# Optimization experiments

Measured on AMD Instinct MI355X. Metric: run time of the kernel, lower is better.

## Reference

```python
import jax, jax.numpy as jnp
import numpy as np
from math import sqrt

N_USERS = 60000
N_ITEMS = 40000
D = 64
B = 3
LAYERS = 2
E = 600000
BATCH = 2048
N_NODES = (N_USERS + 1) + (N_ITEMS + 1)
REG_WEIGHT = 1e-3
BPR_GAMMA = 1e-10


def setup_inputs() -> dict:
    key = jax.random.key(0)
    k0, k1, k2, k3, k4 = jax.random.split(key, 5)
    user_emb = jax.random.normal(k0, (N_USERS + 1, D), jnp.float32) * 0.1
    item_emb = jax.random.normal(k1, (N_ITEMS + 1, D), jnp.float32) * 0.1
    W = jnp.ones((B,), jnp.float32)
    edge_users = jax.random.randint(k2, (B, E), 1, N_USERS + 1)
    edge_items = jax.random.randint(k3, (B, E), 1, N_ITEMS + 1)
    batch_data = jax.random.randint(k4, (BATCH, B, 3), 1, N_ITEMS + 1)
    return dict(user_emb=user_emb, item_emb=item_emb, W=W,
                edge_users=edge_users, edge_items=edge_items,
                batch_data=batch_data)


def _lightgcn(emb, eu, ei, layers):
    # bipartite undirected graph: users <-> items (items offset by N_USERS+1)
    it = ei + (N_USERS + 1)
    src = jnp.concatenate([eu, it])
    dst = jnp.concatenate([it, eu])
    deg = jax.ops.segment_sum(jnp.ones_like(src, jnp.float32), src, N_NODES)
    norm = jax.lax.rsqrt(jnp.maximum(deg[src], 1.0)) * jax.lax.rsqrt(jnp.maximum(deg[dst], 1.0))
    out = emb
    cur = emb
    for _ in range(layers):
        cur = jax.ops.segment_sum(cur[src] * norm[:, None], dst, N_NODES)
        out = out + cur
    return out / (layers + 1)


def _mutual_attention(f):
    # f: [N, B, D]
    S = jnp.einsum('nid,njd->nij', f, f)          # [N, B, B] pairwise scores
    last = S[:, B - 1:B, :]                        # [N, 1, B]
    proj = S[:, :B - 1, :]                         # [N, B-1, B]
    # (last * proj) * last / (last^2 + eps)   (dim-1 is size 1, sums/norms trivial)
    clear = (last * proj) * last / (last * last + 1e-12)   # [N, B-1, B]
    scores = jnp.sum(clear, axis=1, keepdims=True) + last   # [N, 1, B]
    all_scores = jnp.concatenate([clear, scores], axis=1)   # [N, B, B]
    att = jax.nn.softmax(all_scores / sqrt(D), axis=-1)
    return jnp.einsum('nij,njd->nid', att, f)


def reference(user_emb, item_emb, W, edge_users, edge_items, batch_data):
    total0 = jnp.concatenate([user_emb, item_emb], axis=0)   # [N_NODES, D]
    # global graph = union of all behaviors
    g_eu = edge_users.reshape(-1)
    g_ei = edge_items.reshape(-1)
    all_emb = _lightgcn(total0, g_eu, g_ei, LAYERS)
    # per-behavior propagation
    u_list, i_list = [], []
    for b in range(B):
        eb = _lightgcn(all_emb, edge_users[b], edge_items[b], LAYERS)
        u_list.append(eb[:N_USERS + 1])
        i_list.append(eb[N_USERS + 1:])
    all_user = jnp.stack(u_list, axis=1)   # [n_users+1, B, D]
    all_item = jnp.stack(i_list, axis=1)   # [n_items+1, B, D]
    all_user = _mutual_attention(all_user)
    # item behaviour degree: interactions per item per behavior
    ones = jnp.ones((E,), jnp.float32)
    ibd = jnp.stack([jax.ops.segment_sum(ones, edge_items[b], N_ITEMS + 1)
                     for b in range(B)], axis=1)   # [n_items+1, B]
    weight = ibd * W
    weight = weight / (jnp.sum(weight, axis=1, keepdims=True) + 1e-8)
    item_final = jnp.sum(all_item * weight[:, :, None], axis=1)   # [n_items+1, D]
    total_loss = jnp.float32(0.0)
    for b in range(B):
        users = batch_data[:, b, 0]
        items = batch_data[:, b, 1:3]
        uf = all_user[:, b][users][:, None, :]      # [batch, 1, D]
        itf = item_final[items]                      # [batch, 2, D]
        scores = jnp.sum(uf * itf, axis=2)           # [batch, 2]
        total_loss = total_loss - jnp.mean(
            jnp.log(BPR_GAMMA + jax.nn.sigmoid(scores[:, 0] - scores[:, 1])))
    emb_loss = (jnp.linalg.norm(user_emb) + jnp.linalg.norm(item_emb)) / (N_ITEMS + 1)
    return total_loss + REG_WEIGHT * emb_loss
```

## Files before the change

### kernel.cpp

```cpp
#include <hip/hip_runtime.h>
#include <hip/hip_bf16.h>
#include <math.h>

#define NUQ 60001
#define NIQ 40001
#define NNQ 100002
#define DQ  64
#define EQ  600000
#define BQ  3
#define BATCHQ 2048
#define ROWW 32
#define RST ((NNQ + 1) * ROWW)
#define NSLOT (BATCHQ * BQ)
#define NPAD 100004
#define ADJB 1200000
#define BLK_ELE 2048
#define NBLK ((NNQ + BLK_ELE - 1) / BLK_ELE)
#define RANGE 392
#define NRANGE 256
#define NBINS (BQ * NRANGE)
#define NBLKA 256
#define EPB ((BQ * EQ + NBLKA - 1) / NBLKA)

__device__ __forceinline__ float wave_sum(float v) {
#pragma unroll
  for (int m = 32; m >= 1; m >>= 1) v += __shfl_xor(v, m, 64);
  return v;
}
__device__ __forceinline__ int wave_sum_i(int v) {
#pragma unroll
  for (int m = 32; m >= 1; m >>= 1) v += __shfl_xor(v, m, 64);
  return v;
}

__device__ __forceinline__ unsigned pack_bf2(float lo, float hi) {
  unsigned a = __float_as_uint(lo);
  unsigned b = __float_as_uint(hi);
  a = (a + 0x7FFFu + ((a >> 16) & 1u)) >> 16;
  b = (b + 0x7FFFu + ((b >> 16) & 1u)) >> 16;
  return a | (b << 16);
}
__device__ __forceinline__ float unpk_lo(unsigned u) { return __uint_as_float(u << 16); }
__device__ __forceinline__ float unpk_hi(unsigned u) { return __uint_as_float(u & 0xFFFF0000u); }

__global__ void zero_i_k(int* __restrict__ p, int n) {
  int tid = blockIdx.x * blockDim.x + threadIdx.x;
  int stride = gridDim.x * blockDim.x;
  for (int i = tid; i < n; i += stride) p[i] = 0;
}

__global__ void sumsq_k(const float* __restrict__ p, int n, float* __restrict__ acc) {
  int tid = blockIdx.x * blockDim.x + threadIdx.x;
  int stride = gridDim.x * blockDim.x;
  float s = 0.f;
  for (int i = tid; i < n; i += stride) { float v = p[i]; s += v * v; }
  s = wave_sum(s);
  __shared__ float ws[4];
  if ((threadIdx.x & 63) == 0) ws[threadIdx.x >> 6] = s;
  __syncthreads();
  if (threadIdx.x == 0) atomicAdd(acc, ws[0] + ws[1] + ws[2] + ws[3]);
}

__global__ void binc_k(const int* __restrict__ eu, const int* __restrict__ ei,
                       unsigned* __restrict__ counts) {
  __shared__ unsigned h[NBINS];
  for (int i = threadIdx.x; i < NBINS; i += 256) h[i] = 0u;
  __syncthreads();
  int base = blockIdx.x * EPB;
  int end = base + EPB;
  if (end > BQ * EQ) end = BQ * EQ;
  for (int idx = base + threadIdx.x; idx < end; idx += 256) {
    int b = idx / EQ;
    int u = eu[idx];
    int it = ei[idx] + NUQ;
    atomicAdd(&h[b * NRANGE + u / RANGE], 1u);
    atomicAdd(&h[b * NRANGE + it / RANGE], 1u);
  }
  __syncthreads();
  for (int i = threadIdx.x; i < NBINS; i += 256)
    counts[(size_t)blockIdx.x * NBINS + i] = h[i];
}

__global__ void binscan1_k(const unsigned* __restrict__ counts,
                           unsigned* __restrict__ offs, unsigned* __restrict__ bintot) {
  int bin = blockIdx.x;
  int t = threadIdx.x;
  int lane = t & 63, wid = t >> 6;
  unsigned v = counts[(size_t)t * NBINS + bin];
  unsigned incl = v;
#pragma unroll
  for (int off = 1; off < 64; off <<= 1) {
    unsigned x = __shfl_up(incl, off, 64);
    if (lane >= off) incl += x;
  }
  __shared__ unsigned wsum[4];
  if (lane == 63) wsum[wid] = incl;
  __syncthreads();
  if (t == 0) {
    unsigned s = 0;
#pragma unroll
    for (int w = 0; w < 4; ++w) { unsigned x = wsum[w]; wsum[w] = s; s += x; }
  }
  __syncthreads();
  unsigned excl = incl - v + wsum[wid];
  offs[(size_t)t * NBINS + bin] = excl;
  if (t == 255) bintot[bin] = excl + v;
}

__global__ void binscan2_k(const unsigned* __restrict__ bintot,
                           unsigned* __restrict__ binstart) {
  int t = threadIdx.x;
  int lane = t & 63, wid = t >> 6;
  unsigned c0 = bintot[t * 3 + 0], c1 = bintot[t * 3 + 1], c2 = bintot[t * 3 + 2];
  unsigned tsum = c0 + c1 + c2;
  unsigned incl = tsum;
#pragma unroll
  for (int off = 1; off < 64; off <<= 1) {
    unsigned x = __shfl_up(incl, off, 64);
    if (lane >= off) incl += x;
  }
  __shared__ unsigned wsum[4];
  if (lane == 63) wsum[wid] = incl;
  __syncthreads();
  if (t == 0) {
    unsigned s = 0;
#pragma unroll
    for (int w = 0; w < 4; ++w) { unsigned x = wsum[w]; wsum[w] = s; s += x; }
  }
  __syncthreads();
  unsigned run = incl - tsum + wsum[wid];
  binstart[t * 3 + 0] = run; run += c0;
  binstart[t * 3 + 1] = run; run += c1;
  binstart[t * 3 + 2] = run; run += c2;
  if (t == 255) binstart[NBINS] = run;
}

__global__ void binfill_k(const int* __restrict__ eu, const int* __restrict__ ei,
                          const unsigned* __restrict__ offs,
                          const unsigned* __restrict__ binstart,
                          unsigned* __restrict__ records) {
  __shared__ unsigned cur[NBINS];
  for (int i = threadIdx.x; i < NBINS; i += 256)
    cur[i] = binstart[i] + offs[(size_t)blockIdx.x * NBINS + i];
  __syncthreads();
  int base = blockIdx.x * EPB;
  int end = base + EPB;
  if (end > BQ * EQ) end = BQ * EQ;
  for (int idx = base + threadIdx.x; idx < end; idx += 256) {
    int b = idx / EQ;
    int u = eu[idx];
    int itl = ei[idx];
    int it = itl + NUQ;
    unsigned p = atomicAdd(&cur[b * NRANGE + u / RANGE], 1u);
    records[p] = ((unsigned)(u % RANGE) << 16) | (unsigned)itl;
    unsigned q = atomicAdd(&cur[b * NRANGE + it / RANGE], 1u);
    records[q] = ((unsigned)(it % RANGE) << 16) | (unsigned)u;
  }
}

__global__ void bindeg_k(const unsigned* __restrict__ records,
                         const unsigned* __restrict__ binstart,
                         int* __restrict__ degB) {
  int bin = blockIdx.x;
  int b = bin / NRANGE;
  int r0 = (bin % NRANGE) * RANGE;
  __shared__ int h[RANGE];
  for (int i = threadIdx.x; i < RANGE; i += 256) h[i] = 0;
  __syncthreads();
  unsigned rs = binstart[bin], re = binstart[bin + 1];
  for (unsigned j = rs + threadIdx.x; j < re; j += 256)
    atomicAdd(&h[records[j] >> 16], 1);
  __syncthreads();
  int nval = NNQ - r0;
  if (nval > RANGE) nval = RANGE;
  int* deg = degB + (size_t)b * NPAD;
  for (int i = threadIdx.x; i < nval; i += 256) deg[r0 + i] = h[i];
}

__global__ void scan_p1_k(const int* __restrict__ degB, int* __restrict__ partial) {
  int b = blockIdx.x / NBLK;
  int blk = blockIdx.x % NBLK;
  const int* deg = degB + (size_t)b * NPAD;
  int base = blk * BLK_ELE + threadIdx.x * 8;
  int s = 0;
#pragma unroll
  for (int i = 0; i < 8; ++i) { int idx = base + i; if (idx < NNQ) s += deg[idx]; }
  s = wave_sum_i(s);
  __shared__ int lds[4];
  int wid = threadIdx.x >> 6;
  if ((threadIdx.x & 63) == 0) lds[wid] = s;
  __syncthreads();
  if (threadIdx.x == 0) partial[b * NBLK + blk] = lds[0] + lds[1] + lds[2] + lds[3];
}

__global__ void scan_p2_k(int* __restrict__ partial, int* __restrict__ rowptrB) {
  int wid = threadIdx.x >> 6;
  int lane = threadIdx.x & 63;
  if (wid >= BQ) return;
  int v = (lane < NBLK) ? partial[wid * NBLK + lane] : 0;
  int orig = v;
#pragma unroll
  for (int off = 1; off < 64; off <<= 1) {
    int t = __shfl_up(v, off, 64);
    if (lane >= off) v += t;
  }
  if (lane < NBLK) partial[wid * NBLK + lane] = v - orig;
  if (lane == NBLK - 1) rowptrB[(size_t)wid * NPAD + NNQ] = v;
}

__global__ void scan_p3_k(const int* __restrict__ degB, const int* __restrict__ partial,
                          int* __restrict__ rowptrB, float* __restrict__ invsqB) {
  int b = blockIdx.x / NBLK;
  int blk = blockIdx.x % NBLK;
  const int* deg = degB + (size_t)b * NPAD;
  int* rowptr = rowptrB + (size_t)b * NPAD;
  float* invsq = invsqB + (size_t)b * NPAD;
  int base = blk * BLK_ELE + threadIdx.x * 8;
  int d[8];
  int tsum = 0;
#pragma unroll
  for (int i = 0; i < 8; ++i) {
    int idx = base + i;
    d[i] = (idx < NNQ) ? deg[idx] : 0;
    tsum += d[i];
  }
  int lane = threadIdx.x & 63;
  int wid = threadIdx.x >> 6;
  int incl = tsum;
#pragma unroll
  for (int off = 1; off < 64; off <<= 1) {
    int t = __shfl_up(incl, off, 64);
    if (lane >= off) incl += t;
  }
  int excl = incl - tsum;
  __shared__ int lds[4];
  if (lane == 63) lds[wid] = incl;
  __syncthreads();
  if (threadIdx.x == 0) {
    int s = 0;
#pragma unroll
    for (int w = 0; w < 4; ++w) { int t = lds[w]; lds[w] = s; s += t; }
  }
  __syncthreads();
  int run = excl + lds[wid] + partial[b * NBLK + blk];
#pragma unroll
  for (int i = 0; i < 8; ++i) {
    int idx = base + i;
    if (idx < NNQ) {
      rowptr[idx] = run;
      run += d[i];
      invsq[idx] = rsqrtf(fmaxf((float)d[i], 1.f));
    }
  }
}

__global__ void invsqg_k(const int* __restrict__ degB, float* __restrict__ invsqG) {
  int n = blockIdx.x * blockDim.x + threadIdx.x;
  if (n >= NNQ) return;
  int dg = degB[n] + degB[NPAD + n] + degB[2 * NPAD + n];
  invsqG[n] = rsqrtf(fmaxf((float)dg, 1.f));
}

__global__ void binscat_k(const unsigned* __restrict__ records,
                          const unsigned* __restrict__ binstart,
                          const int* __restrict__ rowptrB,
                          unsigned short* __restrict__ adjB) {
  int bin = blockIdx.x;
  int b = bin / NRANGE;
  int r0 = (bin % NRANGE) * RANGE;
  int nval = NNQ - r0;
  if (nval > RANGE) nval = RANGE;
  __shared__ int cur[RANGE];
  const int* rowptr = rowptrB + (size_t)b * NPAD;
  for (int i = threadIdx.x; i < nval; i += 256) cur[i] = rowptr[r0 + i];
  __syncthreads();
  unsigned rs = binstart[bin], re = binstart[bin + 1];
  unsigned short* adj = adjB + (size_t)b * ADJB;
  for (unsigned j = rs + threadIdx.x; j < re; j += 256) {
    unsigned rec = records[j];
    int dl = rec >> 16;
    int pos = atomicAdd(&cur[dl], 1);
    adj[pos] = (unsigned short)(rec & 0xFFFFu);
  }
}

__global__ void pack_emb_k(const float* __restrict__ ue, const float* __restrict__ ie,
                           const float* __restrict__ invsqG,
                           unsigned* __restrict__ E0, unsigned* __restrict__ E0s) {
  int idx = blockIdx.x * blockDim.x + threadIdx.x;
  if (idx >= (NNQ + 1) * ROWW) return;
  int n = idx >> 5, k = idx & 31;
  if (n >= NNQ) { E0s[idx] = 0u; return; }
  const float* src = (n < NUQ) ? (ue + (size_t)n * DQ) : (ie + (size_t)(n - NUQ) * DQ);
  float a = src[2 * k], b = src[2 * k + 1];
  E0[idx] = pack_bf2(a, b);
  float s = invsqG[n];
  E0s[idx] = pack_bf2(a * s, b * s);
}

__device__ __forceinline__ void gather_ns(const unsigned* __restrict__ S,
                                          const unsigned short* __restrict__ adj,
                                          int start, int end, int offs,
                                          int lane, unsigned k4, int g,
                                          float& alo, float& ahi) {
  for (int j0 = start; j0 < end; j0 += 64) {
    int nloc = end - j0;
    if (nloc > 64) nloc = 64;
    unsigned boff = ((unsigned)NNQ) << 7;
    if (lane < nloc) boff = (unsigned)((int)adj[j0 + lane] + offs) << 7;
    for (int j = 0; j < nloc; j += 16) {
#pragma unroll
      for (int m = 0; m < 8; ++m) {
        int jj = j + 2 * m + g;
        unsigned bo = (unsigned)__shfl((int)boff, jj, 64) + k4;
        unsigned dd = *(const unsigned*)((const char*)S + bo);
        alo += unpk_lo(dd);
        ahi += unpk_hi(dd);
      }
    }
  }
}

__device__ __forceinline__ void gather_w(const unsigned* __restrict__ S,
                                         const unsigned short* __restrict__ adj,
                                         const float* __restrict__ invsq,
                                         int start, int end, int offs,
                                         int lane, unsigned k4, int g,
                                         float& alo, float& ahi) {
  for (int j0 = start; j0 < end; j0 += 64) {
    int nloc = end - j0;
    if (nloc > 64) nloc = 64;
    unsigned boff = (unsigned)offs << 7;
    float w = 0.f;
    if (lane < nloc) {
      int a = (int)adj[j0 + lane] + offs;
      boff = (unsigned)a << 7;
      w = invsq[a];
    }
    for (int j = 0; j < nloc; j += 16) {
#pragma unroll
      for (int m = 0; m < 8; ++m) {
        int jj = j + 2 * m + g;
        unsigned bo = (unsigned)__shfl((int)boff, jj, 64) + k4;
        float ww = __shfl(w, jj, 64);
        unsigned dd = *(const unsigned*)((const char*)S + bo);
        alo += ww * unpk_lo(dd);
        ahi += ww * unpk_hi(dd);
      }
    }
  }
}

__global__ void g_l1_k(const unsigned* __restrict__ E0s, unsigned* __restrict__ T1,
                       unsigned* __restrict__ T1s,
                       const int* __restrict__ rowptrB, const unsigned short* __restrict__ adjB,
                       const float* __restrict__ invsqG) {
  int wid = (blockIdx.x * blockDim.x + threadIdx.x) >> 6;
  int lane = threadIdx.x & 63;
  if (wid > NNQ) return;
  int k = lane & 31, g = lane >> 5;
  unsigned k4 = (unsigned)k << 2;
  if (wid == NNQ) { if (lane < 32) T1s[(size_t)wid * ROWW + k] = 0u; return; }
  int offs = (wid < NUQ) ? NUQ : 0;
  float alo = 0.f, ahi = 0.f;
#pragma unroll
  for (int b = 0; b < BQ; ++b) {
    const int* rp = rowptrB + (size_t)b * NPAD;
    gather_ns(E0s, adjB + (size_t)b * ADJB, rp[wid], rp[wid + 1], offs, lane, k4, g, alo, ahi);
  }
  alo += __shfl_xor(alo, 32, 64);
  ahi += __shfl_xor(ahi, 32, 64);
  float s = invsqG[wid];
  if (lane < 32) {
    T1[(size_t)wid * ROWW + k] = pack_bf2(alo * s, ahi * s);
    T1s[(size_t)wid * ROWW + k] = pack_bf2(alo * s * s, ahi * s * s);
  }
}

__global__ void g_l2c_k(const unsigned* __restrict__ E0, const unsigned* __restrict__ T1,
                        const unsigned* __restrict__ T1s,
                        unsigned* __restrict__ C, unsigned* __restrict__ Cs,
                        const int* __restrict__ rowptrB, const unsigned short* __restrict__ adjB,
                        const float* __restrict__ invsqG, const float* __restrict__ invsqB) {
  int wid = (blockIdx.x * blockDim.x + threadIdx.x) >> 6;
  int lane = threadIdx.x & 63;
  if (wid > NNQ) return;
  int k = lane & 31, g = lane >> 5;
  unsigned k4 = (unsigned)k << 2;
  if (wid == NNQ) {
    if (lane < 32) {
#pragma unroll
      for (int b = 0; b < BQ; ++b) Cs[(size_t)b * RST + (size_t)wid * ROWW + k] = 0u;
    }
    return;
  }
  int offs = (wid < NUQ) ? NUQ : 0;
  float alo = 0.f, ahi = 0.f;
#pragma unroll
  for (int b = 0; b < BQ; ++b) {
    const int* rp = rowptrB + (size_t)b * NPAD;
    gather_ns(T1s, adjB + (size_t)b * ADJB, rp[wid], rp[wid + 1], offs, lane, k4, g, alo, ahi);
  }
  alo += __shfl_xor(alo, 32, 64);
  ahi += __shfl_xor(ahi, 32, 64);
  if (lane < 32) {
    float s = invsqG[wid];
    unsigned e0 = E0[(size_t)wid * ROWW + k];
    unsigned t1 = T1[(size_t)wid * ROWW + k];
    float clo = (unpk_lo(e0) + unpk_lo(t1) + alo * s) * (1.f / 3.f);
    float chi = (unpk_hi(e0) + unpk_hi(t1) + ahi * s) * (1.f / 3.f);
    C[(size_t)wid * ROWW + k] = pack_bf2(clo, chi);
#pragma unroll
    for (int b = 0; b < BQ; ++b) {
      float sb = invsqB[(size_t)b * NPAD + wid];
      Cs[(size_t)b * RST + (size_t)wid * ROWW + k] = pack_bf2(clo * sb, chi * sb);
    }
  }
}

__global__ void b_l1_k(const unsigned* __restrict__ Csb, unsigned* __restrict__ T1Bb,
                       const int* __restrict__ rowptr, const unsigned short* __restrict__ adj,
                       const float* __restrict__ ivb) {
  int wid = (blockIdx.x * blockDim.x + threadIdx.x) >> 6;
  int lane = threadIdx.x & 63;
  if (wid >= NNQ) return;
  int k = lane & 31, g = lane >> 5;
  unsigned k4 = (unsigned)k << 2;
  int offs = (wid < NUQ) ? NUQ : 0;
  float alo = 0.f, ahi = 0.f;
  gather_ns(Csb, adj, rowptr[wid], rowptr[wid + 1], offs, lane, k4, g, alo, ahi);
  alo += __shfl_xor(alo, 32, 64);
  ahi += __shfl_xor(ahi, 32, 64);
  float s = ivb[wid];
  if (lane < 32)
    T1Bb[(size_t)wid * ROWW + k] = pack_bf2(alo * s, ahi * s);
}

__global__ void slot_users_k(const unsigned* __restrict__ C, const unsigned* __restrict__ T1B,
                             const int* __restrict__ rowptrB, const unsigned short* __restrict__ adjB,
                             const float* __restrict__ invsqB,
                             const int* __restrict__ batch, float* __restrict__ UG) {
  int slot = (blockIdx.x * blockDim.x + threadIdx.x) >> 6;
  int lane = threadIdx.x & 63;
  if (slot >= NSLOT) return;
  int b = blockIdx.y;
  const int* rp = rowptrB + (size_t)b * NPAD;
  const float* iv = invsqB + (size_t)b * NPAD;
  const unsigned* T1 = T1B + (size_t)b * NNQ * ROWW;
  int u = batch[slot * 3 + 0];
  int k = lane & 31, g = lane >> 5;
  unsigned k4 = (unsigned)k << 2;
  float alo = 0.f, ahi = 0.f;
  gather_w(T1, adjB + (size_t)b * ADJB, iv, rp[u], rp[u + 1], NUQ, lane, k4, g, alo, ahi);
  alo += __shfl_xor(alo, 32, 64);
  ahi += __shfl_xor(ahi, 32, 64);
  float s = iv[u];
  unsigned c0 = C[(size_t)u * ROWW + k];
  unsigned t0 = T1[(size_t)u * ROWW + k];
  if (lane < 32) {
    size_t base = ((size_t)slot * BQ + b) * DQ;
    UG[base + 2 * k]     = (unpk_lo(c0) + unpk_lo(t0) + alo * s) * (1.f / 3.f);
    UG[base + 2 * k + 1] = (unpk_hi(c0) + unpk_hi(t0) + ahi * s) * (1.f / 3.f);
  }
}

__global__ void slot_items_k(const unsigned* __restrict__ C, const unsigned* __restrict__ T1B,
                             const int* __restrict__ rowptrB, const unsigned short* __restrict__ adjB,
                             const float* __restrict__ invsqB,
                             const int* __restrict__ batch, float* __restrict__ IG) {
  int islot = (blockIdx.x * blockDim.x + threadIdx.x) >> 6;
  int lane = threadIdx.x & 63;
  if (islot >= 2 * NSLOT) return;
  int b = blockIdx.y;
  const int* rp = rowptrB + (size_t)b * NPAD;
  const float* iv = invsqB + (size_t)b * NPAD;
  const unsigned* T1 = T1B + (size_t)b * NNQ * ROWW;
  int slot = islot >> 1;
  int c = (islot & 1) + 1;
  int n = batch[slot * 3 + c] + NUQ;
  int k = lane & 31, g = lane >> 5;
  unsigned k4 = (unsigned)k << 2;
  float alo = 0.f, ahi = 0.f;
  gather_w(T1, adjB + (size_t)b * ADJB, iv, rp[n], rp[n + 1], 0, lane, k4, g, alo, ahi);
  alo += __shfl_xor(alo, 32, 64);
  ahi += __shfl_xor(ahi, 32, 64);
  float s = iv[n];
  unsigned c0 = C[(size_t)n * ROWW + k];
  unsigned t0 = T1[(size_t)n * ROWW + k];
  if (lane < 32) {
    size_t base = ((size_t)islot * BQ + b) * DQ;
    IG[base + 2 * k]     = (unpk_lo(c0) + unpk_lo(t0) + alo * s) * (1.f / 3.f);
    IG[base + 2 * k + 1] = (unpk_hi(c0) + unpk_hi(t0) + ahi * s) * (1.f / 3.f);
  }
}

__global__ void epilogue_k(const float* __restrict__ UG, const float* __restrict__ IG,
                           const int* __restrict__ degB, const int* __restrict__ batch,
                           const float* __restrict__ W, float* __restrict__ acc) {
  int slot = (blockIdx.x * blockDim.x + threadIdx.x) >> 6;
  int lane = threadIdx.x & 63;
  float val = 0.f;
  if (slot < NSLOT) {
    int bb = slot % BQ;
    size_t base = (size_t)slot * (BQ * DQ) + lane;
    float a0 = UG[base], a1 = UG[base + 64], a2 = UG[base + 128];
    float p00 = wave_sum(a0 * a0);
    float p01 = wave_sum(a0 * a1);
    float p02 = wave_sum(a0 * a2);
    float p11 = wave_sum(a1 * a1);
    float p12 = wave_sum(a1 * a2);
    float p22 = wave_sum(a2 * a2);
    float last[3] = {p02, p12, p22};
    float S0[3] = {p00, p01, p02};
    float S1[3] = {p01, p11, p12};
    float rows[3][3];
#pragma unroll
    for (int j = 0; j < 3; ++j) {
      float l = last[j];
      float f = l * l / (l * l + 1e-12f);
      float c0 = S0[j] * f;
      float c1 = S1[j] * f;
      rows[0][j] = c0;
      rows[1][j] = c1;
      rows[2][j] = c0 + c1 + l;
    }
    float x0 = rows[bb][0] * 0.125f, x1 = rows[bb][1] * 0.125f, x2 = rows[bb][2] * 0.125f;
    float m = fmaxf(x0, fmaxf(x1, x2));
    float e0 = expf(x0 - m), e1 = expf(x1 - m), e2 = expf(x2 - m);
    float inv = 1.f / (e0 + e1 + e2);
    float uf = (e0 * a0 + e1 * a1 + e2 * a2) * inv;
    float sco[2];
#pragma unroll
    for (int c = 0; c < 2; ++c) {
      int islot = slot * 2 + c;
      int node = batch[slot * 3 + 1 + c] + NUQ;
      float w0 = (float)degB[0 * NPAD + node] * W[0];
      float w1 = (float)degB[1 * NPAD + node] * W[1];
      float w2 = (float)degB[2 * NPAD + node] * W[2];
      float inv2 = 1.f / (w0 + w1 + w2 + 1e-8f);
      size_t rb = (size_t)islot * (BQ * DQ) + lane;
      float ifv = (IG[rb] * w0 + IG[rb + 64] * w1 + IG[rb + 128] * w2) * inv2;
      sco[c] = wave_sum(uf * ifv);
    }
    if (lane == 0) {
      float x = sco[0] - sco[1];
      float sg = 1.f / (1.f + expf(-x));
      val = -logf(1e-10f + sg) * (1.f / (float)BATCHQ);
    }
  }
  __shared__ float ws[4];
  if (lane == 0) ws[threadIdx.x >> 6] = val;
  __syncthreads();
  if (threadIdx.x == 0) atomicAdd(acc, ws[0] + ws[1] + ws[2] + ws[3]);
}

__global__ void finalize_k(const float* __restrict__ sc, unsigned int* __restrict__ out) {
  float total = sc[0] + 0.001f * (sqrtf(sc[1]) + sqrtf(sc[2])) / (float)NIQ;
  unsigned int bits = __float_as_uint(total);
  unsigned int lsb = (bits >> 16) & 1u;
  unsigned int rb = (bits + 0x7FFFu + lsb) >> 16;
  out[0] = (rb << 16) | rb;
}

extern "C" void kernel_launch(void* const* d_in, const int* in_sizes, int n_in,
                              void* d_out, int out_size, void* d_ws, size_t ws_size,
                              hipStream_t stream) {
  const float* ue = (const float*)d_in[0];
  const float* ie = (const float*)d_in[1];
  const float* W  = (const float*)d_in[2];
  const int* eu    = (const int*)d_in[3];
  const int* ei    = (const int*)d_in[4];
  const int* batch = (const int*)d_in[5];

  unsigned* E0  = (unsigned*)d_ws;
  unsigned* E0s = E0 + (size_t)NNQ * ROWW;
  unsigned* T1  = E0s + (size_t)RST;
  unsigned* T1s = T1 + (size_t)NNQ * ROWW;
  unsigned* C   = T1s + (size_t)RST;
  unsigned* Cs  = C + (size_t)NNQ * ROWW;
  unsigned* T1B = Cs + (size_t)BQ * RST;
  float* UG   = (float*)(T1B + (size_t)BQ * NNQ * ROWW);
  float* IG   = UG + (size_t)NSLOT * (BQ * DQ);
  unsigned short* adjB = (unsigned short*)(IG + (size_t)2 * NSLOT * (BQ * DQ));
  int* rowptrB= (int*)(adjB + (size_t)BQ * ADJB);
  int* degB   = rowptrB + 3 * NPAD;
  float* invsqB = (float*)(degB + 3 * NPAD);
  float* invsqG = invsqB + 3 * NPAD;
  unsigned* counts = (unsigned*)(invsqG + NPAD);
  unsigned* offs   = counts + (size_t)NBLKA * NBINS;
  unsigned* bintot = offs + (size_t)NBLKA * NBINS;
  unsigned* binstart = bintot + 1024;
  unsigned* records = binstart + 1024;
  int* partial  = (int*)(records + (size_t)2 * BQ * EQ);
  float* sc   = (float*)(partial + 256);

  zero_i_k<<<1, 64, 0, stream>>>((int*)sc, 8);
  sumsq_k<<<512, 256, 0, stream>>>(ue, NUQ * DQ, sc + 1);
  sumsq_k<<<512, 256, 0, stream>>>(ie, NIQ * DQ, sc + 2);

  binc_k<<<NBLKA, 256, 0, stream>>>(eu, ei, counts);
  binscan1_k<<<NBINS, 256, 0, stream>>>(counts, offs, bintot);
  binscan2_k<<<1, 256, 0, stream>>>(bintot, binstart);
  binfill_k<<<NBLKA, 256, 0, stream>>>(eu, ei, offs, binstart, records);
  bindeg_k<<<NBINS, 256, 0, stream>>>(records, binstart, degB);
  scan_p1_k<<<BQ * NBLK, 256, 0, stream>>>(degB, partial);
  scan_p2_k<<<1, 256, 0, stream>>>(partial, rowptrB);
  scan_p3_k<<<BQ * NBLK, 256, 0, stream>>>(degB, partial, rowptrB, invsqB);
  invsqg_k<<<(NNQ + 255) / 256, 256, 0, stream>>>(degB, invsqG);
  binscat_k<<<NBINS, 256, 0, stream>>>(records, binstart, rowptrB, adjB);

  pack_emb_k<<<((NNQ + 1) * ROWW + 255) / 256, 256, 0, stream>>>(ue, ie, invsqG, E0, E0s);

  const int NODE_BLKS1 = (NNQ + 1 + 3) / 4;
  const int NODE_BLKS = (NNQ + 3) / 4;

  g_l1_k<<<NODE_BLKS1, 256, 0, stream>>>(E0s, T1, T1s, rowptrB, adjB, invsqG);
  g_l2c_k<<<NODE_BLKS1, 256, 0, stream>>>(E0, T1, T1s, C, Cs, rowptrB, adjB, invsqG, invsqB);

  for (int b = 0; b < BQ; ++b) {
    b_l1_k<<<NODE_BLKS, 256, 0, stream>>>(Cs + (size_t)b * RST,
                                          T1B + (size_t)b * NNQ * ROWW,
                                          rowptrB + (size_t)b * NPAD,
                                          adjB + (size_t)b * ADJB,
                                          invsqB + (size_t)b * NPAD);
  }

  slot_users_k<<<dim3((NSLOT + 3) / 4, 3), 256, 0, stream>>>(C, T1B, rowptrB, adjB, invsqB, batch, UG);
  slot_items_k<<<dim3((2 * NSLOT + 3) / 4, 3), 256, 0, stream>>>(C, T1B, rowptrB, adjB, invsqB, batch, IG);
  epilogue_k<<<(NSLOT + 3) / 4, 256, 0, stream>>>(UG, IG, degB, batch, W, sc);
  finalize_k<<<1, 1, 0, stream>>>(sc, (unsigned int*)d_out);
}
```

Measured before the change: 478.5 us.

## Merge per-behavior neighbor gathers and use nontemporal loads/stores for streamed buffers

```diff
diff --git a/kernel.cpp b/kernel.cpp
--- a/kernel.cpp
+++ b/kernel.cpp
@@ -43,6 +43,11 @@
 __device__ __forceinline__ float unpk_lo(unsigned u) { return __uint_as_float(u << 16); }
 __device__ __forceinline__ float unpk_hi(unsigned u) { return __uint_as_float(u & 0xFFFF0000u); }
 
+__device__ __forceinline__ void ntst_u32(unsigned* p, unsigned v) { __builtin_nontemporal_store(v, p); }
+__device__ __forceinline__ void ntst_f32(float* p, float v) { __builtin_nontemporal_store(v, p); }
+__device__ __forceinline__ unsigned ntld_u32(const unsigned* p) { return __builtin_nontemporal_load(p); }
+__device__ __forceinline__ float ntld_f32(const float* p) { return __builtin_nontemporal_load(p); }
+
 __global__ void zero_i_k(int* __restrict__ p, int n) {
   int tid = blockIdx.x * blockDim.x + threadIdx.x;
   int stride = gridDim.x * blockDim.x;
@@ -293,9 +298,9 @@
   if (n >= NNQ) { E0s[idx] = 0u; return; }
   const float* src = (n < NUQ) ? (ue + (size_t)n * DQ) : (ie + (size_t)(n - NUQ) * DQ);
   float a = src[2 * k], b = src[2 * k + 1];
-  E0[idx] = pack_bf2(a, b);
+  ntst_u32(&E0[idx], pack_bf2(a, b));
   float s = invsqG[n];
-  E0s[idx] = pack_bf2(a * s, b * s);
+  ntst_u32(&E0s[idx], pack_bf2(a * s, b * s));
 }
 
 __device__ __forceinline__ void gather_ns(const unsigned* __restrict__ S,
@@ -308,6 +313,39 @@
     if (nloc > 64) nloc = 64;
     unsigned boff = ((unsigned)NNQ) << 7;
     if (lane < nloc) boff = (unsigned)((int)adj[j0 + lane] + offs) << 7;
+    for (int j = 0; j < nloc; j += 16) {
+#pragma unroll
+      for (int m = 0; m < 8; ++m) {
+        int jj = j + 2 * m + g;
+        unsigned bo = (unsigned)__shfl((int)boff, jj, 64) + k4;
+        unsigned dd = *(const unsigned*)((const char*)S + bo);
+        alo += unpk_lo(dd);
+        ahi += unpk_hi(dd);
+      }
+    }
+  }
+}
+
+__device__ __forceinline__ void gather3(const unsigned* __restrict__ S,
+                                        const unsigned short* __restrict__ adjB,
+                                        int s0, int d0, int s1, int d1,
+                                        int s2, int d2, int offs,
+                                        int lane, unsigned k4, int g,
+                                        float& alo, float& ahi) {
+  int D = d0 + d1 + d2;
+  int d01 = d0 + d1;
+  for (int j0 = 0; j0 < D; j0 += 64) {
+    int nloc = D - j0;
+    if (nloc > 64) nloc = 64;
+    unsigned boff = ((unsigned)NNQ) << 7;
+    int l = j0 + lane;
+    if (l < D) {
+      int idx;
+      if (l < d0)       idx = s0 + l;
+      else if (l < d01) idx = ADJB + s1 + (l - d0);
+      else              idx = 2 * ADJB + s2 + (l - d01);
+      boff = (unsigned)((int)adjB[idx] + offs) << 7;
+    }
     for (int j = 0; j < nloc; j += 16) {
 #pragma unroll
       for (int m = 0; m < 8; ++m) {
@@ -362,18 +400,20 @@
   unsigned k4 = (unsigned)k << 2;
   if (wid == NNQ) { if (lane < 32) T1s[(size_t)wid * ROWW + k] = 0u; return; }
   int offs = (wid < NUQ) ? NUQ : 0;
+  const int* rp0 = rowptrB;
+  const int* rp1 = rowptrB + NPAD;
+  const int* rp2 = rowptrB + 2 * (size_t)NPAD;
+  int s0 = rp0[wid], d0 = rp0[wid + 1] - s0;
+  int s1 = rp1[wid], d1 = rp1[wid + 1] - s1;
+  int s2 = rp2[wid], d2 = rp2[wid + 1] - s2;
   float alo = 0.f, ahi = 0.f;
-#pragma unroll
-  for (int b = 0; b < BQ; ++b) {
-    const int* rp = rowptrB + (size_t)b * NPAD;
-    gather_ns(E0s, adjB + (size_t)b * ADJB, rp[wid], rp[wid + 1], offs, lane, k4, g, alo, ahi);
-  }
+  gather3(E0s, adjB, s0, d0, s1, d1, s2, d2, offs, lane, k4, g, alo, ahi);
   alo += __shfl_xor(alo, 32, 64);
   ahi += __shfl_xor(ahi, 32, 64);
   float s = invsqG[wid];
   if (lane < 32) {
-    T1[(size_t)wid * ROWW + k] = pack_bf2(alo * s, ahi * s);
-    T1s[(size_t)wid * ROWW + k] = pack_bf2(alo * s * s, ahi * s * s);
+    ntst_u32(&T1[(size_t)wid * ROWW + k], pack_bf2(alo * s, ahi * s));
+    ntst_u32(&T1s[(size_t)wid * ROWW + k], pack_bf2(alo * s * s, ahi * s * s));
   }
 }
 
@@ -395,25 +435,27 @@
     return;
   }
   int offs = (wid < NUQ) ? NUQ : 0;
+  const int* rp0 = rowptrB;
+  const int* rp1 = rowptrB + NPAD;
+  const int* rp2 = rowptrB + 2 * (size_t)NPAD;
+  int s0 = rp0[wid], d0 = rp0[wid + 1] - s0;
+  int s1 = rp1[wid], d1 = rp1[wid + 1] - s1;
+  int s2 = rp2[wid], d2 = rp2[wid + 1] - s2;
   float alo = 0.f, ahi = 0.f;
-#pragma unroll
-  for (int b = 0; b < BQ; ++b) {
-    const int* rp = rowptrB + (size_t)b * NPAD;
-    gather_ns(T1s, adjB + (size_t)b * ADJB, rp[wid], rp[wid + 1], offs, lane, k4, g, alo, ahi);
-  }
+  gather3(T1s, adjB, s0, d0, s1, d1, s2, d2, offs, lane, k4, g, alo, ahi);
   alo += __shfl_xor(alo, 32, 64);
   ahi += __shfl_xor(ahi, 32, 64);
   if (lane < 32) {
     float s = invsqG[wid];
-    unsigned e0 = E0[(size_t)wid * ROWW + k];
-    unsigned t1 = T1[(size_t)wid * ROWW + k];
+    unsigned e0 = ntld_u32(&E0[(size_t)wid * ROWW + k]);
+    unsigned t1 = ntld_u32(&T1[(size_t)wid * ROWW + k]);
     float clo = (unpk_lo(e0) + unpk_lo(t1) + alo * s) * (1.f / 3.f);
     float chi = (unpk_hi(e0) + unpk_hi(t1) + ahi * s) * (1.f / 3.f);
-    C[(size_t)wid * ROWW + k] = pack_bf2(clo, chi);
+    ntst_u32(&C[(size_t)wid * ROWW + k], pack_bf2(clo, chi));
 #pragma unroll
     for (int b = 0; b < BQ; ++b) {
       float sb = invsqB[(size_t)b * NPAD + wid];
-      Cs[(size_t)b * RST + (size_t)wid * ROWW + k] = pack_bf2(clo * sb, chi * sb);
+      ntst_u32(&Cs[(size_t)b * RST + (size_t)wid * ROWW + k], pack_bf2(clo * sb, chi * sb));
     }
   }
 }
@@ -433,7 +475,7 @@
   ahi += __shfl_xor(ahi, 32, 64);
   float s = ivb[wid];
   if (lane < 32)
-    T1Bb[(size_t)wid * ROWW + k] = pack_bf2(alo * s, ahi * s);
+    ntst_u32(&T1Bb[(size_t)wid * ROWW + k], pack_bf2(alo * s, ahi * s));
 }
 
 __global__ void slot_users_k(const unsigned* __restrict__ C, const unsigned* __restrict__ T1B,
@@ -459,8 +501,8 @@
   unsigned t0 = T1[(size_t)u * ROWW + k];
   if (lane < 32) {
     size_t base = ((size_t)slot * BQ + b) * DQ;
-    UG[base + 2 * k]     = (unpk_lo(c0) + unpk_lo(t0) + alo * s) * (1.f / 3.f);
-    UG[base + 2 * k + 1] = (unpk_hi(c0) + unpk_hi(t0) + ahi * s) * (1.f / 3.f);
+    ntst_f32(&UG[base + 2 * k],     (unpk_lo(c0) + unpk_lo(t0) + alo * s) * (1.f / 3.f));
+    ntst_f32(&UG[base + 2 * k + 1], (unpk_hi(c0) + unpk_hi(t0) + ahi * s) * (1.f / 3.f));
   }
 }
 
@@ -489,8 +531,8 @@
   unsigned t0 = T1[(size_t)n * ROWW + k];
   if (lane < 32) {
     size_t base = ((size_t)islot * BQ + b) * DQ;
-    IG[base + 2 * k]     = (unpk_lo(c0) + unpk_lo(t0) + alo * s) * (1.f / 3.f);
-    IG[base + 2 * k + 1] = (unpk_hi(c0) + unpk_hi(t0) + ahi * s) * (1.f / 3.f);
+    ntst_f32(&IG[base + 2 * k],     (unpk_lo(c0) + unpk_lo(t0) + alo * s) * (1.f / 3.f));
+    ntst_f32(&IG[base + 2 * k + 1], (unpk_hi(c0) + unpk_hi(t0) + ahi * s) * (1.f / 3.f));
   }
 }
 
@@ -503,7 +545,9 @@
   if (slot < NSLOT) {
     int bb = slot % BQ;
     size_t base = (size_t)slot * (BQ * DQ) + lane;
-    float a0 = UG[base], a1 = UG[base + 64], a2 = UG[base + 128];
+    float a0 = ntld_f32(&UG[base]);
+    float a1 = ntld_f32(&UG[base + 64]);
+    float a2 = ntld_f32(&UG[base + 128]);
     float p00 = wave_sum(a0 * a0);
     float p01 = wave_sum(a0 * a1);
     float p02 = wave_sum(a0 * a2);
@@ -539,7 +583,8 @@
       float w2 = (float)degB[2 * NPAD + node] * W[2];
       float inv2 = 1.f / (w0 + w1 + w2 + 1e-8f);
       size_t rb = (size_t)islot * (BQ * DQ) + lane;
-      float ifv = (IG[rb] * w0 + IG[rb + 64] * w1 + IG[rb + 128] * w2) * inv2;
+      float ifv = (ntld_f32(&IG[rb]) * w0 + ntld_f32(&IG[rb + 64]) * w1 +
+                   ntld_f32(&IG[rb + 128]) * w2) * inv2;
       sco[c] = wave_sum(uf * ifv);
     }
     if (lane == 0) {
```

Result: faster. 466.4 us (-2.5%).
